# Performance work log

Hardware: AMD Instinct MI355X
Metric: run time of the kernel (lower is better)

The kernel has to match this reference:

```python
import jax, jax.numpy as jnp
import numpy as np

BETA = 0.95
THR = 1.0

@jax.custom_vjp
def spike(v):
    return (v > 0).astype(v.dtype)

def _spike_fwd(v):
    return (v > 0).astype(v.dtype), v

def _spike_bwd(v, g):
    # snntorch ATan surrogate (alpha=2): dH/dv ~ 1 / (1 + (pi*v)^2)
    return (g / (1.0 + (jnp.pi * v) ** 2),)

spike.defvjp(_spike_fwd, _spike_bwd)

def conv1x1(x, w, b):
    # 1x1 conv == channel contraction
    return jnp.einsum('bchw,oc->bohw', x, w) + b[None, :, None, None]

def pool2(x):
    B, C, H, W = x.shape
    return x.reshape(B, C, H // 2, 2, W // 2, 2).max(axis=(3, 5))

def lif_step(mem, spk_prev, cur):
    # snntorch Leaky (reset_mechanism='subtract'): reset uses previous step's
    # detached spike, then fire on the new membrane.
    new_mem = BETA * mem + cur - jax.lax.stop_gradient(spk_prev) * THR
    spk = spike(new_mem - THR)
    return new_mem, spk

def setup_inputs():
    key = jax.random.key(0)
    ks = jax.random.split(key, 8)
    T, B, H, W = 10, 8, 256, 320
    def w(k, o, i):
        return jax.random.normal(k, (o, i), jnp.float32) / np.sqrt(i)
    return {
        'x': jax.random.normal(ks[0], (T, B, 2, H, W), jnp.float32),
        'w1': w(ks[1], 32, 2),   'b1': jnp.zeros((32,), jnp.float32),
        'w2': w(ks[2], 64, 32),  'b2': jnp.zeros((64,), jnp.float32),
        'w3': w(ks[3], 64, 64),  'b3': jnp.zeros((64,), jnp.float32),
        'w4': w(ks[4], 128, 64), 'b4': jnp.zeros((128,), jnp.float32),
        'w5': w(ks[5], 128, 128),'b5': jnp.zeros((128,), jnp.float32),
        'fc1_w': jax.random.normal(ks[6], (4096, 10240), jnp.float32) / np.sqrt(10240),
        'fc1_b': jnp.zeros((4096,), jnp.float32),
        'fc2_w': jax.random.normal(ks[7], (4, 4096), jnp.float32) / np.sqrt(4096),
        'fc2_b': jnp.zeros((4,), jnp.float32),
    }

def reference(x, w1, b1, w2, b2, w3, b3, w4, b4, w5, b5, fc1_w, fc1_b, fc2_w, fc2_b):
    T, B, _, H, W = x.shape
    convs = ((w1, b1), (w2, b2), (w3, b3), (w4, b4), (w5, b5))
    chans = (32, 64, 64, 128, 128)
    # layer i sees input pooled i times -> membrane at (H>>i, W>>i)
    mems = tuple(jnp.zeros((B, chans[i], H >> i, W >> i), x.dtype) for i in range(5))
    spks = tuple(jnp.zeros_like(m) for m in mems)

    def step(carry, xt):
        mems, spks = carry
        h = xt
        new_mems, new_spks = [], []
        for i, (wi, bi) in enumerate(convs):
            cur = conv1x1(h, wi, bi)
            m, s = lif_step(mems[i], spks[i], cur)
            new_mems.append(m)
            new_spks.append(s)
            h = pool2(s)
        return (tuple(new_mems), tuple(new_spks)), h  # h: [B,128,8,10]

    _, spk_rec = jax.lax.scan(step, (mems, spks), x)  # [T,B,128,8,10]

    # FIL head: sum spikes over time, then one pass through Linear+LIF stack.
    # Hidden states start at zero, so mem = beta*0 + cur = cur at this single step.
    s = spk_rec.sum(axis=0).reshape(B, -1)   # [B, 10240]
    mem1 = s @ fc1_w.T + fc1_b
    spk1 = spike(mem1 - THR)
    mem2 = spk1 @ fc2_w.T + fc2_b            # reset_mechanism='none', mem returned
    return mem2                               # [B, 4]
```

## Files before the change

### kernel.cpp

```cpp
#include <hip/hip_runtime.h>
#include <stdint.h>

#define BETA 0.95f
#define THR  1.0f

__device__ __forceinline__ float bitf(uint32_t w, int sh) {
  return (float)((w >> sh) & 1u);
}

__global__ __launch_bounds__(64) void k_l1(const float* __restrict__ x,
                                           const float* __restrict__ w1,
                                           const float* __restrict__ b1,
                                           uint32_t* __restrict__ S1) {
  const int u  = blockIdx.x * 64 + threadIdx.x;
  const int q  = u >> 2;
  const int dx = u & 1, dy = (u >> 1) & 1;
  const int pw = q % 160;
  const int ph = (q / 160) % 128;
  const int b  = q / (160 * 128);
  const int row = 2 * ph + dy;
  const int col = 2 * pw + dx;

  float m[32];
#pragma unroll
  for (int o = 0; o < 32; ++o) m[o] = 0.f;

#pragma unroll 1
  for (int t = 0; t < 10; ++t) {
    const size_t tb = (size_t)(t * 8 + b) * 2 * 81920 + (size_t)row * 320 + col;
    const float x0 = x[tb];
    const float x1 = x[tb + 81920];
    uint32_t mask = 0u;
#pragma unroll
    for (int o = 0; o < 32; ++o) {
      const float cur = fmaf(w1[o * 2 + 1], x1, fmaf(w1[o * 2], x0, b1[o]));
      float mo = m[o];
      const float rst = (mo > THR) ? THR : 0.f;
      mo = fmaf(BETA, mo, cur) - rst;
      m[o] = mo;
      mask |= (mo > THR) ? (1u << o) : 0u;
    }
    mask |= __shfl_xor(mask, 1, 64);
    mask |= __shfl_xor(mask, 2, 64);
    if ((threadIdx.x & 3) == 0)
      S1[((size_t)(t * 8 + b) * 128 + ph) * 160 + pw] = mask;
  }
}

__global__ __launch_bounds__(64) void k_l2(const uint32_t* __restrict__ S1,
                                           const float* __restrict__ w2,
                                           const float* __restrict__ b2,
                                           uint8_t* __restrict__ S2) {
  const int g = blockIdx.x & 7;
  const int patch = (blockIdx.x >> 3) * 64 + threadIdx.x;
  const int pw = patch % 80;
  const int py = (patch / 80) % 64;
  const int b  = patch / (80 * 64);

  float m[4][8];
#pragma unroll
  for (int p = 0; p < 4; ++p)
#pragma unroll
    for (int o = 0; o < 8; ++o) m[p][o] = 0.f;

#pragma unroll 1
  for (int t = 0; t < 10; ++t) {
    uint32_t msk[4];
#pragma unroll
    for (int dy = 0; dy < 2; ++dy) {
      const uint2 v = *(const uint2*)(S1 +
        ((size_t)(t * 8 + b) * 128 + 2 * py + dy) * 160 + 2 * pw);
      msk[dy * 2 + 0] = v.x;
      msk[dy * 2 + 1] = v.y;
    }
    float cur[4][8];
#pragma unroll
    for (int p = 0; p < 4; ++p)
#pragma unroll
      for (int oo = 0; oo < 8; ++oo) cur[p][oo] = b2[g * 8 + oo];
#pragma unroll
    for (int cq = 0; cq < 8; ++cq) {
      float sp[4][4];
#pragma unroll
      for (int p = 0; p < 4; ++p)
#pragma unroll
        for (int j = 0; j < 4; ++j) sp[p][j] = bitf(msk[p], 4 * cq + j);
#pragma unroll
      for (int oo = 0; oo < 8; ++oo) {
        const float4 wv = *(const float4*)(w2 + ((g * 8 + oo) * 32 + 4 * cq));
#pragma unroll
        for (int p = 0; p < 4; ++p) {
          float a = cur[p][oo];
          a = fmaf(wv.x, sp[p][0], a);
          a = fmaf(wv.y, sp[p][1], a);
          a = fmaf(wv.z, sp[p][2], a);
          a = fmaf(wv.w, sp[p][3], a);
          cur[p][oo] = a;
        }
      }
    }
    uint32_t pooled = 0u;
#pragma unroll
    for (int oo = 0; oo < 8; ++oo)
#pragma unroll
      for (int p = 0; p < 4; ++p) {
        float mo = m[p][oo];
        const float rst = (mo > THR) ? THR : 0.f;
        mo = fmaf(BETA, mo, cur[p][oo]) - rst;
        m[p][oo] = mo;
        pooled |= (mo > THR) ? (1u << oo) : 0u;
      }
    S2[((size_t)((t * 8 + b) * 64 + py) * 80 + pw) * 8 + g] = (uint8_t)pooled;
  }
}

__global__ __launch_bounds__(64) void k_l3(const uint8_t* __restrict__ S2,
                                           const float* __restrict__ w3,
                                           const float* __restrict__ b3,
                                           uint8_t* __restrict__ S3) {
  const int g = blockIdx.x & 7;
  const int posu = (blockIdx.x >> 3) * 64 + threadIdx.x;
  const int qq = posu >> 2;
  const int dx = posu & 1, dy = (posu >> 1) & 1;
  const int px = qq % 40;
  const int py = (qq / 40) % 32;
  const int b  = qq / 1280;
  const int row = 2 * py + dy;
  const int col = 2 * px + dx;

  float m[8];
#pragma unroll
  for (int o = 0; o < 8; ++o) m[o] = 0.f;

#pragma unroll 1
  for (int t = 0; t < 10; ++t) {
    const uint2 v = *(const uint2*)(S2 +
      ((size_t)((t * 8 + b) * 64 + row) * 80 + col) * 8);
    const uint32_t lo = v.x, hi = v.y;

    float cur[8];
#pragma unroll
    for (int oo = 0; oo < 8; ++oo) cur[oo] = b3[g * 8 + oo];
#pragma unroll
    for (int cq = 0; cq < 16; ++cq) {
      float sp[4];
#pragma unroll
      for (int j = 0; j < 4; ++j)
        sp[j] = bitf((cq < 8) ? lo : hi, (4 * cq + j) & 31);
#pragma unroll
      for (int oo = 0; oo < 8; ++oo) {
        const float4 wv = *(const float4*)(w3 + ((g * 8 + oo) * 64 + 4 * cq));
        float a = cur[oo];
        a = fmaf(wv.x, sp[0], a);
        a = fmaf(wv.y, sp[1], a);
        a = fmaf(wv.z, sp[2], a);
        a = fmaf(wv.w, sp[3], a);
        cur[oo] = a;
      }
    }
    uint32_t pooled = 0u;
#pragma unroll
    for (int oo = 0; oo < 8; ++oo) {
      float mo = m[oo];
      const float rst = (mo > THR) ? THR : 0.f;
      mo = fmaf(BETA, mo, cur[oo]) - rst;
      m[oo] = mo;
      pooled |= (mo > THR) ? (1u << oo) : 0u;
    }
    pooled |= __shfl_xor(pooled, 1, 64);
    pooled |= __shfl_xor(pooled, 2, 64);
    if ((threadIdx.x & 3) == 0)
      S3[((size_t)((t * 8 + b) * 32 + py) * 40 + px) * 8 + g] = (uint8_t)pooled;
  }
}

__global__ __launch_bounds__(64) void k_l4(const uint8_t* __restrict__ S3,
                                           const float* __restrict__ w4,
                                           const float* __restrict__ b4,
                                           uint8_t* __restrict__ S4) {
  const int g = blockIdx.x & 15;
  const int posu = (blockIdx.x >> 4) * 64 + threadIdx.x;
  const int qq = posu >> 2;
  const int dx = posu & 1, dy = (posu >> 1) & 1;
  const int px = qq % 20;
  const int py = (qq / 20) % 16;
  const int b  = qq / 320;
  const int row = 2 * py + dy;
  const int col = 2 * px + dx;

  float m[8];
#pragma unroll
  for (int o = 0; o < 8; ++o) m[o] = 0.f;

#pragma unroll 1
  for (int t = 0; t < 10; ++t) {
    const uint2 v = *(const uint2*)(S3 +
      ((size_t)((t * 8 + b) * 32 + row) * 40 + col) * 8);
    const uint32_t lo = v.x, hi = v.y;

    float cur[8];
#pragma unroll
    for (int oo = 0; oo < 8; ++oo) cur[oo] = b4[g * 8 + oo];
#pragma unroll
    for (int cq = 0; cq < 16; ++cq) {
      float sp[4];
#pragma unroll
      for (int j = 0; j < 4; ++j)
        sp[j] = bitf((cq < 8) ? lo : hi, (4 * cq + j) & 31);
#pragma unroll
      for (int oo = 0; oo < 8; ++oo) {
        const float4 wv = *(const float4*)(w4 + ((g * 8 + oo) * 64 + 4 * cq));
        float a = cur[oo];
        a = fmaf(wv.x, sp[0], a);
        a = fmaf(wv.y, sp[1], a);
        a = fmaf(wv.z, sp[2], a);
        a = fmaf(wv.w, sp[3], a);
        cur[oo] = a;
      }
    }
    uint32_t pooled = 0u;
#pragma unroll
    for (int oo = 0; oo < 8; ++oo) {
      float mo = m[oo];
      const float rst = (mo > THR) ? THR : 0.f;
      mo = fmaf(BETA, mo, cur[oo]) - rst;
      m[oo] = mo;
      pooled |= (mo > THR) ? (1u << oo) : 0u;
    }
    pooled |= __shfl_xor(pooled, 1, 64);
    pooled |= __shfl_xor(pooled, 2, 64);
    if ((threadIdx.x & 3) == 0)
      S4[((size_t)((t * 8 + b) * 16 + py) * 20 + px) * 16 + g] = (uint8_t)pooled;
  }
}

__global__ __launch_bounds__(64) void k_l5(const uint8_t* __restrict__ S4,
                                           const float* __restrict__ w5,
                                           const float* __restrict__ b5,
                                           float* __restrict__ s) {
  const int g = blockIdx.x & 15;
  const int posu = (blockIdx.x >> 4) * 64 + threadIdx.x;
  const int qq = posu >> 2;
  const int dx = posu & 1, dy = (posu >> 1) & 1;
  const int px = qq % 10;
  const int py = (qq / 10) % 8;
  const int b  = qq / 80;
  const int row = 2 * py + dy;
  const int col = 2 * px + dx;

  float m[8], scnt[8];
#pragma unroll
  for (int o = 0; o < 8; ++o) { m[o] = 0.f; scnt[o] = 0.f; }

#pragma unroll 1
  for (int t = 0; t < 10; ++t) {
    const uint4 v = *(const uint4*)(S4 +
      ((size_t)((t * 8 + b) * 16 + row) * 20 + col) * 16);
    uint32_t wrd[4] = {v.x, v.y, v.z, v.w};

    float cur[8];
#pragma unroll
    for (int oo = 0; oo < 8; ++oo) cur[oo] = b5[g * 8 + oo];
#pragma unroll
    for (int cq = 0; cq < 32; ++cq) {
      float sp[4];
#pragma unroll
      for (int j = 0; j < 4; ++j)
        sp[j] = bitf(wrd[cq >> 3], (cq & 7) * 4 + j);
#pragma unroll
      for (int oo = 0; oo < 8; ++oo) {
        const float4 wv = *(const float4*)(w5 + ((g * 8 + oo) * 128 + 4 * cq));
        float a = cur[oo];
        a = fmaf(wv.x, sp[0], a);
        a = fmaf(wv.y, sp[1], a);
        a = fmaf(wv.z, sp[2], a);
        a = fmaf(wv.w, sp[3], a);
        cur[oo] = a;
      }
    }
    uint32_t pooled = 0u;
#pragma unroll
    for (int oo = 0; oo < 8; ++oo) {
      float mo = m[oo];
      const float rst = (mo > THR) ? THR : 0.f;
      mo = fmaf(BETA, mo, cur[oo]) - rst;
      m[oo] = mo;
      pooled |= (mo > THR) ? (1u << oo) : 0u;
    }
    pooled |= __shfl_xor(pooled, 1, 64);
    pooled |= __shfl_xor(pooled, 2, 64);
#pragma unroll
    for (int oo = 0; oo < 8; ++oo) scnt[oo] += bitf(pooled, oo);
  }
  if ((threadIdx.x & 3) == 0) {
#pragma unroll
    for (int oo = 0; oo < 8; ++oo)
      s[b * 10240 + (g * 8 + oo) * 80 + py * 10 + px] = scnt[oo];
  }
}

__global__ __launch_bounds__(64) void k_fc1(const float* __restrict__ s,
                                            const float* __restrict__ W,
                                            float* __restrict__ pt) {
  const int lane = threadIdx.x;
  const int o8 = blockIdx.x & 511;
  const int kq = blockIdx.x >> 9;

  float acc[8][8];
#pragma unroll
  for (int os = 0; os < 8; ++os)
#pragma unroll
    for (int bb = 0; bb < 8; ++bb) acc[os][bb] = 0.f;

#pragma unroll 1
  for (int it = 0; it < 10; ++it) {
    const int k = kq * 2560 + it * 256 + lane * 4;
    float4 sv[8];
#pragma unroll
    for (int bb = 0; bb < 8; ++bb) sv[bb] = *(const float4*)(s + bb * 10240 + k);
#pragma unroll
    for (int os = 0; os < 8; ++os) {
      const float4 wv = *(const float4*)(W + (size_t)(o8 * 8 + os) * 10240 + k);
#pragma unroll
      for (int bb = 0; bb < 8; ++bb) {
        float a = acc[os][bb];
        a = fmaf(wv.x, sv[bb].x, a);
        a = fmaf(wv.y, sv[bb].y, a);
        a = fmaf(wv.z, sv[bb].z, a);
        a = fmaf(wv.w, sv[bb].w, a);
        acc[os][bb] = a;
      }
    }
  }
#pragma unroll
  for (int os = 0; os < 8; ++os)
#pragma unroll
    for (int bb = 0; bb < 8; ++bb) {
      float v = acc[os][bb];
#pragma unroll
      for (int mq = 1; mq < 64; mq <<= 1) v += __shfl_xor(v, mq, 64);
      acc[os][bb] = v;
    }
  float out = 0.f;
#pragma unroll
  for (int os = 0; os < 8; ++os)
#pragma unroll
    for (int bb = 0; bb < 8; ++bb)
      out = (lane == os * 8 + bb) ? acc[os][bb] : out;
  const int os = lane >> 3;
  const int bb = lane & 7;
  pt[((kq * 8 + bb) * 4096) + o8 * 8 + os] = out;
}

__global__ __launch_bounds__(64) void k_fc2(const float* __restrict__ pt,
                                            const float* __restrict__ fc1_b,
                                            const float* __restrict__ fc2_w,
                                            const float* __restrict__ fc2_b,
                                            float* __restrict__ out) {
  const int lane = threadIdx.x;
  const int b = blockIdx.x >> 2;
  const int j = blockIdx.x & 3;
  float acc = 0.f;
#pragma unroll 4
  for (int it = 0; it < 64; ++it) {
    const int o = it * 64 + lane;
    const float m1 = pt[(0 * 8 + b) * 4096 + o] + pt[(1 * 8 + b) * 4096 + o]
                   + pt[(2 * 8 + b) * 4096 + o] + pt[(3 * 8 + b) * 4096 + o]
                   + fc1_b[o];
    acc += (m1 > THR) ? fc2_w[j * 4096 + o] : 0.f;
  }
#pragma unroll
  for (int mq = 1; mq < 64; mq <<= 1) acc += __shfl_xor(acc, mq, 64);
  if (lane == 0) out[b * 4 + j] = acc + fc2_b[j];
}

extern "C" void kernel_launch(void* const* d_in, const int* in_sizes, int n_in,
                              void* d_out, int out_size, void* d_ws, size_t ws_size,
                              hipStream_t stream) {
  const float* x     = (const float*)d_in[0];
  const float* w1    = (const float*)d_in[1];
  const float* b1    = (const float*)d_in[2];
  const float* w2    = (const float*)d_in[3];
  const float* b2    = (const float*)d_in[4];
  const float* w3    = (const float*)d_in[5];
  const float* b3    = (const float*)d_in[6];
  const float* w4    = (const float*)d_in[7];
  const float* b4    = (const float*)d_in[8];
  const float* w5    = (const float*)d_in[9];
  const float* b5    = (const float*)d_in[10];
  const float* fc1w  = (const float*)d_in[11];
  const float* fc1b  = (const float*)d_in[12];
  const float* fc2w  = (const float*)d_in[13];
  const float* fc2b  = (const float*)d_in[14];

  uint8_t* ws = (uint8_t*)d_ws;
  uint32_t* S1 = (uint32_t*)(ws + 0);
  uint8_t*  S2 = ws + 6553600;
  uint8_t*  S3 = ws + 9830400;
  uint8_t*  S4 = ws + 10649600;
  float*    sb = (float*)(ws + 11059200);
  float*    pt = (float*)(ws + 11386880);

  k_l1<<<10240, 64, 0, stream>>>(x, w1, b1, S1);
  k_l2<<< 5120, 64, 0, stream>>>(S1, w2, b2, S2);
  k_l3<<< 5120, 64, 0, stream>>>(S2, w3, b3, S3);
  k_l4<<< 2560, 64, 0, stream>>>(S3, w4, b4, S4);
  k_l5<<<  640, 64, 0, stream>>>(S4, w5, b5, sb);
  k_fc1<<<2048, 64, 0, stream>>>(sb, fc1w, pt);
  k_fc2<<<  32, 64, 0, stream>>>(pt, fc1b, fc2w, fc2b, (float*)d_out);
}
```

Measured before the change: 751.9 us.

## Prefetch next timestep inputs and widen channel-group parallelism in late layers

Each layer kernel now loads the next timestep's input spikes or pixels one iteration ahead, to hide global-load latency behind the LIF compute. Layers 4 and 5 split output channels into more groups (32 and 64), so more blocks launch with fewer registers each. The fc1 split-K factor doubles to 8, and the fc2 head becomes a two-stage reduction across more blocks. This adds launches and redundant reads of the input spikes across groups in exchange for more parallelism on the small late layers.

```diff
diff --git a/kernel.cpp b/kernel.cpp
--- a/kernel.cpp
+++ b/kernel.cpp
@@ -20,16 +20,23 @@
   const int b  = q / (160 * 128);
   const int row = 2 * ph + dy;
   const int col = 2 * pw + dx;
+  const size_t base = (size_t)row * 320 + col;
 
   float m[32];
 #pragma unroll
   for (int o = 0; o < 32; ++o) m[o] = 0.f;
 
+  float x0 = x[(size_t)b * 2 * 81920 + base];
+  float x1 = x[(size_t)b * 2 * 81920 + base + 81920];
+
 #pragma unroll 1
   for (int t = 0; t < 10; ++t) {
-    const size_t tb = (size_t)(t * 8 + b) * 2 * 81920 + (size_t)row * 320 + col;
-    const float x0 = x[tb];
-    const float x1 = x[tb + 81920];
+    float x0n = 0.f, x1n = 0.f;
+    if (t < 9) {
+      const size_t tb = (size_t)((t + 1) * 8 + b) * 2 * 81920 + base;
+      x0n = x[tb];
+      x1n = x[tb + 81920];
+    }
     uint32_t mask = 0u;
 #pragma unroll
     for (int o = 0; o < 32; ++o) {
@@ -44,6 +51,7 @@
     mask |= __shfl_xor(mask, 2, 64);
     if ((threadIdx.x & 3) == 0)
       S1[((size_t)(t * 8 + b) * 128 + ph) * 160 + pw] = mask;
+    x0 = x0n; x1 = x1n;
   }
 }
 
@@ -56,6 +64,8 @@
   const int pw = patch % 80;
   const int py = (patch / 80) % 64;
   const int b  = patch / (80 * 64);
+  const size_t base0 = ((size_t)b * 128 + 2 * py) * 160 + 2 * pw;
+  const size_t base1 = base0 + 160;
 
   float m[4][8];
 #pragma unroll
@@ -63,16 +73,19 @@
 #pragma unroll
     for (int o = 0; o < 8; ++o) m[p][o] = 0.f;
 
+  uint2 va = *(const uint2*)(S1 + base0);
+  uint2 vb = *(const uint2*)(S1 + base1);
+
 #pragma unroll 1
   for (int t = 0; t < 10; ++t) {
-    uint32_t msk[4];
-#pragma unroll
-    for (int dy = 0; dy < 2; ++dy) {
-      const uint2 v = *(const uint2*)(S1 +
-        ((size_t)(t * 8 + b) * 128 + 2 * py + dy) * 160 + 2 * pw);
-      msk[dy * 2 + 0] = v.x;
-      msk[dy * 2 + 1] = v.y;
-    }
+    uint2 van = {0, 0}, vbn = {0, 0};
+    if (t < 9) {
+      const size_t off = (size_t)(t + 1) * 8 * 128 * 160;
+      van = *(const uint2*)(S1 + off + base0);
+      vbn = *(const uint2*)(S1 + off + base1);
+    }
+    const uint32_t msk[4] = {va.x, va.y, vb.x, vb.y};
+
     float cur[4][8];
 #pragma unroll
     for (int p = 0; p < 4; ++p)
@@ -111,6 +124,7 @@
         pooled |= (mo > THR) ? (1u << oo) : 0u;
       }
     S2[((size_t)((t * 8 + b) * 64 + py) * 80 + pw) * 8 + g] = (uint8_t)pooled;
+    va = van; vb = vbn;
   }
 }
 
@@ -127,15 +141,18 @@
   const int b  = qq / 1280;
   const int row = 2 * py + dy;
   const int col = 2 * px + dx;
+  const size_t base = ((size_t)(b * 64 + row) * 80 + col) * 8;
 
   float m[8];
 #pragma unroll
   for (int o = 0; o < 8; ++o) m[o] = 0.f;
 
+  uint2 v = *(const uint2*)(S2 + base);
+
 #pragma unroll 1
   for (int t = 0; t < 10; ++t) {
-    const uint2 v = *(const uint2*)(S2 +
-      ((size_t)((t * 8 + b) * 64 + row) * 80 + col) * 8);
+    uint2 vn = {0, 0};
+    if (t < 9) vn = *(const uint2*)(S2 + (size_t)(t + 1) * 8 * 64 * 80 * 8 + base);
     const uint32_t lo = v.x, hi = v.y;
 
     float cur[8];
@@ -171,6 +188,7 @@
     pooled |= __shfl_xor(pooled, 2, 64);
     if ((threadIdx.x & 3) == 0)
       S3[((size_t)((t * 8 + b) * 32 + py) * 40 + px) * 8 + g] = (uint8_t)pooled;
+    v = vn;
   }
 }
 
@@ -178,8 +196,8 @@
                                            const float* __restrict__ w4,
                                            const float* __restrict__ b4,
                                            uint8_t* __restrict__ S4) {
-  const int g = blockIdx.x & 15;
-  const int posu = (blockIdx.x >> 4) * 64 + threadIdx.x;
+  const int g = blockIdx.x & 31;
+  const int posu = (blockIdx.x >> 5) * 64 + threadIdx.x;
   const int qq = posu >> 2;
   const int dx = posu & 1, dy = (posu >> 1) & 1;
   const int px = qq % 20;
@@ -187,20 +205,23 @@
   const int b  = qq / 320;
   const int row = 2 * py + dy;
   const int col = 2 * px + dx;
-
-  float m[8];
-#pragma unroll
-  for (int o = 0; o < 8; ++o) m[o] = 0.f;
+  const size_t base = ((size_t)(b * 32 + row) * 40 + col) * 8;
+
+  float m[4];
+#pragma unroll
+  for (int o = 0; o < 4; ++o) m[o] = 0.f;
+
+  uint2 v = *(const uint2*)(S3 + base);
 
 #pragma unroll 1
   for (int t = 0; t < 10; ++t) {
-    const uint2 v = *(const uint2*)(S3 +
-      ((size_t)((t * 8 + b) * 32 + row) * 40 + col) * 8);
+    uint2 vn = {0, 0};
+    if (t < 9) vn = *(const uint2*)(S3 + (size_t)(t + 1) * 8 * 32 * 40 * 8 + base);
     const uint32_t lo = v.x, hi = v.y;
 
-    float cur[8];
-#pragma unroll
-    for (int oo = 0; oo < 8; ++oo) cur[oo] = b4[g * 8 + oo];
+    float cur[4];
+#pragma unroll
+    for (int oo = 0; oo < 4; ++oo) cur[oo] = b4[g * 4 + oo];
 #pragma unroll
     for (int cq = 0; cq < 16; ++cq) {
       float sp[4];
@@ -208,8 +229,8 @@
       for (int j = 0; j < 4; ++j)
         sp[j] = bitf((cq < 8) ? lo : hi, (4 * cq + j) & 31);
 #pragma unroll
-      for (int oo = 0; oo < 8; ++oo) {
-        const float4 wv = *(const float4*)(w4 + ((g * 8 + oo) * 64 + 4 * cq));
+      for (int oo = 0; oo < 4; ++oo) {
+        const float4 wv = *(const float4*)(w4 + ((g * 4 + oo) * 64 + 4 * cq));
         float a = cur[oo];
         a = fmaf(wv.x, sp[0], a);
         a = fmaf(wv.y, sp[1], a);
@@ -220,7 +241,7 @@
     }
     uint32_t pooled = 0u;
 #pragma unroll
-    for (int oo = 0; oo < 8; ++oo) {
+    for (int oo = 0; oo < 4; ++oo) {
       float mo = m[oo];
       const float rst = (mo > THR) ? THR : 0.f;
       mo = fmaf(BETA, mo, cur[oo]) - rst;
@@ -230,7 +251,8 @@
     pooled |= __shfl_xor(pooled, 1, 64);
     pooled |= __shfl_xor(pooled, 2, 64);
     if ((threadIdx.x & 3) == 0)
-      S4[((size_t)((t * 8 + b) * 16 + py) * 20 + px) * 16 + g] = (uint8_t)pooled;
+      S4[((size_t)((t * 8 + b) * 16 + py) * 20 + px) * 32 + g] = (uint8_t)pooled;
+    v = vn;
   }
 }
 
@@ -238,8 +260,8 @@
                                            const float* __restrict__ w5,
                                            const float* __restrict__ b5,
                                            float* __restrict__ s) {
-  const int g = blockIdx.x & 15;
-  const int posu = (blockIdx.x >> 4) * 64 + threadIdx.x;
+  const int g = blockIdx.x & 63;
+  const int posu = (blockIdx.x >> 6) * 64 + threadIdx.x;
   const int qq = posu >> 2;
   const int dx = posu & 1, dy = (posu >> 1) & 1;
   const int px = qq % 10;
@@ -247,29 +269,35 @@
   const int b  = qq / 80;
   const int row = 2 * py + dy;
   const int col = 2 * px + dx;
-
-  float m[8], scnt[8];
-#pragma unroll
-  for (int o = 0; o < 8; ++o) { m[o] = 0.f; scnt[o] = 0.f; }
+  const size_t base = ((size_t)(b * 16 + row) * 20 + col) * 32;
+
+  float m[2] = {0.f, 0.f}, scnt[2] = {0.f, 0.f};
+
+  uint4 v0 = *(const uint4*)(S4 + base);
+  uint4 v1 = *(const uint4*)(S4 + base + 16);
 
 #pragma unroll 1
   for (int t = 0; t < 10; ++t) {
-    const uint4 v = *(const uint4*)(S4 +
-      ((size_t)((t * 8 + b) * 16 + row) * 20 + col) * 16);
-    uint32_t wrd[4] = {v.x, v.y, v.z, v.w};
-
-    float cur[8];
-#pragma unroll
-    for (int oo = 0; oo < 8; ++oo) cur[oo] = b5[g * 8 + oo];
+    uint4 v0n = {0,0,0,0}, v1n = {0,0,0,0};
+    if (t < 9) {
+      const size_t off = (size_t)(t + 1) * 8 * 16 * 20 * 32;
+      v0n = *(const uint4*)(S4 + off + base);
+      v1n = *(const uint4*)(S4 + off + base + 16);
+    }
+    const uint32_t wrd[8] = {v0.x, v0.y, v0.z, v0.w, v1.x, v1.y, v1.z, v1.w};
+
+    float cur[2];
+#pragma unroll
+    for (int oo = 0; oo < 2; ++oo) cur[oo] = b5[g * 2 + oo];
 #pragma unroll
     for (int cq = 0; cq < 32; ++cq) {
       float sp[4];
 #pragma unroll
       for (int j = 0; j < 4; ++j)
-        sp[j] = bitf(wrd[cq >> 3], (cq & 7) * 4 + j);
-#pragma unroll
-      for (int oo = 0; oo < 8; ++oo) {
-        const float4 wv = *(const float4*)(w5 + ((g * 8 + oo) * 128 + 4 * cq));
+        sp[j] = bitf(wrd[cq >> 2], (cq & 3) * 8 + j);
+#pragma unroll
+      for (int oo = 0; oo < 2; ++oo) {
+        const float4 wv = *(const float4*)(w5 + ((g * 2 + oo) * 128 + 4 * cq));
         float a = cur[oo];
         a = fmaf(wv.x, sp[0], a);
         a = fmaf(wv.y, sp[1], a);
@@ -280,7 +308,7 @@
     }
     uint32_t pooled = 0u;
 #pragma unroll
-    for (int oo = 0; oo < 8; ++oo) {
+    for (int oo = 0; oo < 2; ++oo) {
       float mo = m[oo];
       const float rst = (mo > THR) ? THR : 0.f;
       mo = fmaf(BETA, mo, cur[oo]) - rst;
@@ -290,12 +318,13 @@
     pooled |= __shfl_xor(pooled, 1, 64);
     pooled |= __shfl_xor(pooled, 2, 64);
 #pragma unroll
-    for (int oo = 0; oo < 8; ++oo) scnt[oo] += bitf(pooled, oo);
+    for (int oo = 0; oo < 2; ++oo) scnt[oo] += bitf(pooled, oo);
+    v0 = v0n; v1 = v1n;
   }
   if ((threadIdx.x & 3) == 0) {
 #pragma unroll
-    for (int oo = 0; oo < 8; ++oo)
-      s[b * 10240 + (g * 8 + oo) * 80 + py * 10 + px] = scnt[oo];
+    for (int oo = 0; oo < 2; ++oo)
+      s[b * 10240 + (g * 2 + oo) * 80 + py * 10 + px] = scnt[oo];
   }
 }
 
@@ -313,8 +342,8 @@
     for (int bb = 0; bb < 8; ++bb) acc[os][bb] = 0.f;
 
 #pragma unroll 1
-  for (int it = 0; it < 10; ++it) {
-    const int k = kq * 2560 + it * 256 + lane * 4;
+  for (int it = 0; it < 5; ++it) {
+    const int k = kq * 1280 + it * 256 + lane * 4;
     float4 sv[8];
 #pragma unroll
     for (int bb = 0; bb < 8; ++bb) sv[bb] = *(const float4*)(s + bb * 10240 + k);
@@ -352,26 +381,40 @@
   pt[((kq * 8 + bb) * 4096) + o8 * 8 + os] = out;
 }
 
-__global__ __launch_bounds__(64) void k_fc2(const float* __restrict__ pt,
-                                            const float* __restrict__ fc1_b,
-                                            const float* __restrict__ fc2_w,
+__global__ __launch_bounds__(64) void k_fc2p(const float* __restrict__ pt,
+                                             const float* __restrict__ fc1_b,
+                                             const float* __restrict__ fc2_w,
+                                             float* __restrict__ pt2) {
+  const int lane = threadIdx.x;
+  const int b  = blockIdx.x >> 4;
+  const int j  = (blockIdx.x >> 2) & 3;
+  const int oc = blockIdx.x & 3;
+  float acc = 0.f;
+#pragma unroll 2
+  for (int it = 0; it < 16; ++it) {
+    const int o = oc * 1024 + it * 64 + lane;
+    float m1 = fc1_b[o];
+#pragma unroll
+    for (int kq = 0; kq < 8; ++kq) m1 += pt[(kq * 8 + b) * 4096 + o];
+    acc += (m1 > THR) ? fc2_w[j * 4096 + o] : 0.f;
+  }
+#pragma unroll
+  for (int mq = 1; mq < 64; mq <<= 1) acc += __shfl_xor(acc, mq, 64);
+  if (lane == 0) pt2[blockIdx.x] = acc;
+}
+
+__global__ __launch_bounds__(64) void k_fc3(const float* __restrict__ pt2,
                                             const float* __restrict__ fc2_b,
                                             float* __restrict__ out) {
   const int lane = threadIdx.x;
-  const int b = blockIdx.x >> 2;
-  const int j = blockIdx.x & 3;
-  float acc = 0.f;
-#pragma unroll 4
-  for (int it = 0; it < 64; ++it) {
-    const int o = it * 64 + lane;
-    const float m1 = pt[(0 * 8 + b) * 4096 + o] + pt[(1 * 8 + b) * 4096 + o]
-                   + pt[(2 * 8 + b) * 4096 + o] + pt[(3 * 8 + b) * 4096 + o]
-                   + fc1_b[o];
-    acc += (m1 > THR) ? fc2_w[j * 4096 + o] : 0.f;
-  }
-#pragma unroll
-  for (int mq = 1; mq < 64; mq <<= 1) acc += __shfl_xor(acc, mq, 64);
-  if (lane == 0) out[b * 4 + j] = acc + fc2_b[j];
+  if (lane < 32) {
+    const int b = lane >> 2;
+    const int j = lane & 3;
+    float acc = fc2_b[j];
+#pragma unroll
+    for (int oc = 0; oc < 4; ++oc) acc += pt2[b * 16 + j * 4 + oc];
+    out[b * 4 + j] = acc;
+  }
 }
 
 extern "C" void kernel_launch(void* const* d_in, const int* in_sizes, int n_in,
@@ -394,18 +437,20 @@
   const float* fc2b  = (const float*)d_in[14];
 
   uint8_t* ws = (uint8_t*)d_ws;
-  uint32_t* S1 = (uint32_t*)(ws + 0);
-  uint8_t*  S2 = ws + 6553600;
-  uint8_t*  S3 = ws + 9830400;
-  uint8_t*  S4 = ws + 10649600;
-  float*    sb = (float*)(ws + 11059200);
-  float*    pt = (float*)(ws + 11386880);
-
-  k_l1<<<10240, 64, 0, stream>>>(x, w1, b1, S1);
-  k_l2<<< 5120, 64, 0, stream>>>(S1, w2, b2, S2);
-  k_l3<<< 5120, 64, 0, stream>>>(S2, w3, b3, S3);
-  k_l4<<< 2560, 64, 0, stream>>>(S3, w4, b4, S4);
-  k_l5<<<  640, 64, 0, stream>>>(S4, w5, b5, sb);
-  k_fc1<<<2048, 64, 0, stream>>>(sb, fc1w, pt);
-  k_fc2<<<  32, 64, 0, stream>>>(pt, fc1b, fc2w, fc2b, (float*)d_out);
-}
+  uint32_t* S1  = (uint32_t*)(ws + 0);
+  uint8_t*  S2  = ws + 6553600;
+  uint8_t*  S3  = ws + 9830400;
+  uint8_t*  S4  = ws + 10649600;
+  float*    sb  = (float*)(ws + 11468800);
+  float*    pt  = (float*)(ws + 11796480);
+  float*    pt2 = (float*)(ws + 12845056);
+
+  k_l1 <<<10240, 64, 0, stream>>>(x, w1, b1, S1);
+  k_l2 <<< 5120, 64, 0, stream>>>(S1, w2, b2, S2);
+  k_l3 <<< 5120, 64, 0, stream>>>(S2, w3, b3, S3);
+  k_l4 <<< 5120, 64, 0, stream>>>(S3, w4, b4, S4);
+  k_l5 <<< 2560, 64, 0, stream>>>(S4, w5, b5, sb);
+  k_fc1<<< 4096, 64, 0, stream>>>(sb, fc1w, pt);
+  k_fc2p<<< 128, 64, 0, stream>>>(pt, fc1b, fc2w, pt2);
+  k_fc3<<<    1, 64, 0, stream>>>(pt2, fc2b, (float*)d_out);
+}
```

New measurement: 764.2 us. No clear change (+1.6%).
